# Optimization experiments

Measured on AMD Instinct MI355X. Metric: run time of the kernel, lower is better.

The kernel has to match this reference:

```python
import jax, jax.numpy as jnp
import numpy as np

N, E, F_IN, H, L = 50000, 800000, 128, 256, 3


def setup_inputs() -> dict:
    key = jax.random.key(0)
    ks = jax.random.split(key, 6)
    s = 0.05  # keep activations well-scaled through 3 residual layers
    return {
        "x": jax.random.normal(ks[0], (N, F_IN), jnp.float32),
        "edge_index": jax.random.randint(ks[1], (2, E), 0, N, dtype=jnp.int32),
        "Wp": jax.random.normal(ks[2], (H, F_IN), jnp.float32) * s,
        "bp": jnp.zeros((H,), jnp.float32),
        "Wl": jax.random.normal(ks[3], (L, H, H), jnp.float32) * s,
        "bl": jnp.zeros((L, H), jnp.float32),
        "Wr": jax.random.normal(ks[4], (L, H, H), jnp.float32) * s,
        "gamma": jnp.ones((L, H), jnp.float32),
        "beta": jnp.zeros((L, H), jnp.float32),
    }


def _layernorm(x, g, b, eps=1e-5):
    mu = jnp.mean(x, axis=-1, keepdims=True)
    var = jnp.var(x, axis=-1, keepdims=True)
    return (x - mu) * jax.lax.rsqrt(var + eps) * g + b


def reference(x, edge_index, Wp, bp, Wl, bl, Wr, gamma, beta):
    n = x.shape[0]
    src, dst = edge_index[0], edge_index[1]
    # input projection + ReLU
    h = jax.nn.relu(x @ Wp.T + bp)  # [N, H]
    # mean-aggregation normalizer (PyG SAGEConv 'mean'): zero-degree nodes -> 0
    deg = jax.ops.segment_sum(jnp.ones_like(dst, jnp.float32), dst, num_segments=n)
    inv_deg = (1.0 / jnp.maximum(deg, 1.0))[:, None]  # [N, 1]
    num_layers = Wl.shape[0]
    for i in range(num_layers):
        res = h
        # SAGEConv: lin_l(mean of source-neighbor messages) + lin_r(self)
        agg = jax.ops.segment_sum(h[src], dst, num_segments=n) * inv_deg  # [N, H]
        h = agg @ Wl[i].T + bl[i] + h @ Wr[i].T
        # LayerNorm -> ReLU -> (dropout: eval-mode identity) -> residual
        h = jax.nn.relu(_layernorm(h, gamma[i], beta[i])) + res
    return h
```

## Files before the change

### kernel.cpp

```cpp
#include <hip/hip_runtime.h>

#define NN 50000
#define EE 800000
#define FIN 128
#define HH 256
#define NL 3

#define BM 128
#define BK 32
#define TB (16384 + 8192)

typedef __bf16 bf16x8 __attribute__((ext_vector_type(8)));
typedef float  f32x4  __attribute__((ext_vector_type(4)));
typedef unsigned short u16x8 __attribute__((ext_vector_type(8)));

__device__ __forceinline__ float bf2f(unsigned short u){
    union { unsigned int i; float f; } v; v.i = ((unsigned int)u) << 16; return v.f;
}
__device__ __forceinline__ unsigned short f2bf(float f){
    union { float f; unsigned int i; } v; v.f = f;
    unsigned int r = v.i + 0x7FFF + ((v.i >> 16) & 1);
    return (unsigned short)(r >> 16);
}
__device__ __forceinline__ void gload16(const void* g, void* s){
    __builtin_amdgcn_global_load_lds(
        (const __attribute__((address_space(1))) void*)g,
        (__attribute__((address_space(3))) void*)s, 16, 0, 0);
}
__device__ __forceinline__ int permslot(int n){
    return (n & ~63) | ((n & 3) << 4) | ((n >> 2) & 15);
}

__global__ void k_zero_i32(int* __restrict__ p, int n){
    int i = blockIdx.x*256 + threadIdx.x;
    if (i < n) p[i] = 0;
}
__global__ void k_count_deg(const int* __restrict__ dst, int* __restrict__ deg){
    int i = blockIdx.x*256 + threadIdx.x;
    if (i < EE) atomicAdd(&deg[dst[i]], 1);
}
__global__ void k_block_sum(const int* __restrict__ deg, int* __restrict__ bsum){
    __shared__ int s[1024];
    int i = blockIdx.x*1024 + threadIdx.x;
    s[threadIdx.x] = (i < NN) ? deg[i] : 0;
    __syncthreads();
    for (int o = 512; o > 0; o >>= 1){
        if (threadIdx.x < o) s[threadIdx.x] += s[threadIdx.x + o];
        __syncthreads();
    }
    if (threadIdx.x == 0) bsum[blockIdx.x] = s[0];
}
__global__ void k_make_off(const int* __restrict__ deg, const int* __restrict__ bsum,
                           int nb, int* __restrict__ off, int* __restrict__ pos,
                           float* __restrict__ invd){
    __shared__ int s[1024];
    __shared__ int base;
    int t = threadIdx.x;
    if (t < 64){
        int v = (t < blockIdx.x && t < nb) ? bsum[t] : 0;
        #pragma unroll
        for (int m = 1; m <= 32; m <<= 1) v += __shfl_xor(v, m);
        if (t == 0) base = v;
    }
    int i = blockIdx.x*1024 + t;
    int v0 = (i < NN) ? deg[i] : 0;
    s[t] = v0; __syncthreads();
    for (int o = 1; o < 1024; o <<= 1){
        int add = (t >= o) ? s[t - o] : 0;
        __syncthreads();
        s[t] += add;
        __syncthreads();
    }
    if (i < NN){
        int excl = s[t] - v0 + base;
        off[i] = excl; pos[i] = excl;
        invd[i] = 1.0f / fmaxf((float)v0, 1.0f);
    }
}
__global__ __launch_bounds__(256) void k_build_csr(
    const int* __restrict__ src, const int* __restrict__ dst,
    int* __restrict__ pos, int* __restrict__ csr)
{
    const int grp = blockIdx.x & 7;
    const int bin = blockIdx.x >> 3;
    const int nbk = gridDim.x >> 3;
    const int lo  = grp * (NN/8);
    const int hi  = (grp == 7) ? NN : lo + (NN/8);
    for (int i = bin*256 + threadIdx.x; i < EE; i += nbk*256){
        int d = dst[i];
        if (d >= lo && d < hi){
            int p = atomicAdd(&pos[d], 1);
            csr[p] = src[i];
        }
    }
}

#define NX  (NN*FIN/4)
#define NWP (HH*FIN/4)
#define NWC (NL*HH*2*HH/4)
__global__ void k_prep(const float* __restrict__ x, const float* __restrict__ Wp,
                       const float* __restrict__ Wl, const float* __restrict__ Wr,
                       unsigned short* __restrict__ Xb, unsigned short* __restrict__ Wpb,
                       unsigned short* __restrict__ Wb){
    int i = blockIdx.x*256 + threadIdx.x;
    if (i < NX){
        float4 v = *(const float4*)&x[i*4];
        ushort4 o; o.x=f2bf(v.x); o.y=f2bf(v.y); o.z=f2bf(v.z); o.w=f2bf(v.w);
        *(ushort4*)&Xb[i*4] = o;
        return;
    }
    int j = i - NX;
    if (j < NWP){
        int base = j*4;
        int kk = base & (FIN-1);
        int n  = base >> 7;
        float4 v = *(const float4*)&Wp[base];
        ushort4 o; o.x=f2bf(v.x); o.y=f2bf(v.y); o.z=f2bf(v.z); o.w=f2bf(v.w);
        *(ushort4*)&Wpb[permslot(n)*FIN + kk] = o;
        return;
    }
    int k4 = j - NWP;
    if (k4 < NWC){
        int base = k4*4;
        int kk  = base & 511;
        int n   = (base >> 9) & (HH-1);
        int lyr = base >> 17;
        const float* srcp = (kk < HH) ? &Wl[((size_t)lyr*HH + n)*HH + kk]
                                      : &Wr[((size_t)lyr*HH + n)*HH + (kk - HH)];
        float4 v = *(const float4*)srcp;
        ushort4 o; o.x=f2bf(v.x); o.y=f2bf(v.y); o.z=f2bf(v.z); o.w=f2bf(v.w);
        *(ushort4*)&Wb[(size_t)lyr*HH*2*HH + permslot(n)*2*HH + kk] = o;
    }
}

__device__ __forceinline__ void accum16(float* a, uint4 v, float c){
    const unsigned int w0 = v.x, w1 = v.y, w2 = v.z, w3 = v.w;
    #pragma unroll
    for (int b = 0; b < 4; ++b){
        a[b]    += c * (float)((w0 >> (8*b)) & 0xFF);
        a[4+b]  += c * (float)((w1 >> (8*b)) & 0xFF);
        a[8+b]  += c * (float)((w2 >> (8*b)) & 0xFF);
        a[12+b] += c * (float)((w3 >> (8*b)) & 0xFF);
    }
}

__global__ __launch_bounds__(256) void k_aggregate_u8(
    const unsigned char* __restrict__ hu, const float* __restrict__ scl,
    const int* __restrict__ csr, const int* __restrict__ off,
    const int* __restrict__ deg, const float* __restrict__ invd,
    unsigned short* __restrict__ aggb)
{
    const int wave = threadIdx.x >> 6, lane = threadIdx.x & 63;
    const int node = blockIdx.x*4 + wave;
    if (node >= NN) return;
    const int o = off[node], d = deg[node];
    const int grp = lane >> 4;
    const int fl  = lane & 15;

    float acc[16] = {};
    int j = 0;
    for (; j + 16 <= d; j += 16){
        int s0 = csr[o + j      + grp];
        int s1 = csr[o + j + 4  + grp];
        int s2 = csr[o + j + 8  + grp];
        int s3 = csr[o + j + 12 + grp];
        float c0 = scl[s0], c1 = scl[s1], c2 = scl[s2], c3 = scl[s3];
        uint4 v0 = *(const uint4*)&hu[(size_t)s0*HH + fl*16];
        uint4 v1 = *(const uint4*)&hu[(size_t)s1*HH + fl*16];
        uint4 v2 = *(const uint4*)&hu[(size_t)s2*HH + fl*16];
        uint4 v3 = *(const uint4*)&hu[(size_t)s3*HH + fl*16];
        accum16(acc, v0, c0); accum16(acc, v1, c1);
        accum16(acc, v2, c2); accum16(acc, v3, c3);
    }
    for (; j + 8 <= d; j += 8){
        int s0 = csr[o + j     + grp];
        int s1 = csr[o + j + 4 + grp];
        float c0 = scl[s0], c1 = scl[s1];
        uint4 v0 = *(const uint4*)&hu[(size_t)s0*HH + fl*16];
        uint4 v1 = *(const uint4*)&hu[(size_t)s1*HH + fl*16];
        accum16(acc, v0, c0); accum16(acc, v1, c1);
    }
    for (; j < d; j += 4){
        int idx = j + grp;
        int s0 = 0; float c0 = 0.f;
        if (idx < d){ s0 = csr[o + idx]; c0 = scl[s0]; }
        uint4 v0 = *(const uint4*)&hu[(size_t)s0*HH + fl*16];
        accum16(acc, v0, c0);
    }
    #pragma unroll
    for (int k = 0; k < 16; ++k){
        acc[k] += __shfl_xor(acc[k], 16);
        acc[k] += __shfl_xor(acc[k], 32);
    }
    if (grp == 0){
        float id = invd[node];
        u16x8 r0, r1;
        #pragma unroll
        for (int k = 0; k < 8; ++k){
            r0[k] = f2bf(acc[k]*id);
            r1[k] = f2bf(acc[8+k]*id);
        }
        *(u16x8*)&aggb[(size_t)node*HH + fl*16]     = r0;
        *(u16x8*)&aggb[(size_t)node*HH + fl*16 + 8] = r1;
    }
}

template<int EPI>
__global__ __launch_bounds__(1024) void k_gemm_mfma(
    const unsigned short* __restrict__ A0, int lda0,
    const unsigned short* __restrict__ A1, int lda1,
    const unsigned short* __restrict__ Bt,
    const float* __restrict__ bias,
    const float* __restrict__ gamma, const float* __restrict__ beta,
    const unsigned short* __restrict__ resb,
    float* __restrict__ outf, unsigned short* __restrict__ outb,
    unsigned char* __restrict__ hu, float* __restrict__ scl,
    int K0, int KTOT)
{
    __shared__ char smem[3*TB];
    const int t    = threadIdx.x;
    const int w    = t >> 6, l = t & 63;
    const int lr   = l & 15, lg = l >> 4;
    const int half = w >> 3;
    const int wh   = w & 7;
    const int wm   = wh >> 2, wn = wh & 3;
    const int m0h  = blockIdx.x * BM + half*64;

    const int rowB = t >> 2;
    const int swzB = ((t & 3)*16) ^ ((rowB & 6) << 3);
    const char* bsrc = (const char*)(Bt + (size_t)rowB*KTOT) + swzB;
    const int bdstB = t*16;
    const int ua   = t & 255;
    const int rowA = ua >> 2;
    const int swzA = ((ua & 3)*16) ^ ((rowA & 6) << 3);
    int growA = m0h + rowA; if (growA > NN-1) growA = NN-1;
    const char* a0src = (const char*)(A0 + (size_t)growA*lda0) + swzA;
    const char* a1src = (const char*)(A1 + (size_t)growA*lda1) + swzA;
    const int adst = 16384 + half*4096 + ua*16;
    const bool hasA = (wh < 4);

    f32x4 acc[2][4] = {};

    auto stage = [&](int s, int buf){
        const int k0 = s * BK;
        char* base = smem + buf*TB;
        if (hasA){
            const char* g = (k0 < K0) ? (a0src + (size_t)k0*2)
                                      : (a1src + (size_t)(k0 - K0)*2);
            gload16(g, base + adst);
        }
        gload16(bsrc + (size_t)k0*2, base + bdstB);
    };

    const int nsteps = KTOT / BK;
    stage(0, 0);
    int buf = 0;
    for (int s = 0; s < nsteps; ++s){
        int nbuf = (buf == 2) ? 0 : buf + 1;
        if (s + 1 < nsteps){
            stage(s + 1, nbuf);
            if (hasA) { asm volatile("s_waitcnt vmcnt(2)" ::: "memory"); }
            else      { asm volatile("s_waitcnt vmcnt(1)" ::: "memory"); }
        } else {
            asm volatile("s_waitcnt vmcnt(0)" ::: "memory");
        }
        __builtin_amdgcn_s_barrier();
        __builtin_amdgcn_sched_barrier(0);

        const char* As = smem + buf*TB + 16384 + half*4096;
        const char* Bs = smem + buf*TB;
        const int kb = lg * 16;
        const int sw = (lr & 6) << 3;
        bf16x8 af[2], bfr[4];
        #pragma unroll
        for (int m = 0; m < 2; ++m){
            int r = wm*32 + m*16 + lr;
            af[m] = *(const bf16x8*)(As + r*64 + (kb ^ sw));
        }
        #pragma unroll
        for (int n = 0; n < 4; ++n){
            int r = wn*64 + n*16 + lr;
            bfr[n] = *(const bf16x8*)(Bs + r*64 + (kb ^ sw));
        }
        #pragma unroll
        for (int m = 0; m < 2; ++m)
            #pragma unroll
            for (int n = 0; n < 4; ++n)
                acc[m][n] = __builtin_amdgcn_mfma_f32_16x16x32_bf16(af[m], bfr[n], acc[m][n], 0, 0, 0);

        buf = nbuf;
    }
    __syncthreads();

    const int cb = wn*64 + lr*4;
    float4 bq = *(const float4*)&bias[cb];
    float bcol[4] = {bq.x, bq.y, bq.z, bq.w};
    float gcol[4], becol[4];
    if (EPI >= 1){
        float4 gq = *(const float4*)&gamma[cb];
        float4 eq = *(const float4*)&beta[cb];
        gcol[0]=gq.x; gcol[1]=gq.y; gcol[2]=gq.z; gcol[3]=gq.w;
        becol[0]=eq.x; becol[1]=eq.y; becol[2]=eq.z; becol[3]=eq.w;
    }

    float* red  = (float*)(smem + half*4096);
    float* red2 = red + 512;
    float pmx[2][4];

    if (EPI == 0){
        #pragma unroll
        for (int m = 0; m < 2; ++m)
        #pragma unroll
        for (int reg = 0; reg < 4; ++reg){
            int R = wm*32 + m*16 + lg*4 + reg;
            int grow = m0h + R;
            float mx = 0.f;
            ushort4 hb4;
            #pragma unroll
            for (int n = 0; n < 4; ++n){
                float v = fmaxf(acc[m][n][reg] + bcol[n], 0.f);
                acc[m][n][reg] = v;
                mx = fmaxf(mx, v);
                ((unsigned short*)&hb4)[n] = f2bf(v);
            }
            if (grow < NN) *(ushort4*)&outb[(size_t)grow*HH + cb] = hb4;
            pmx[m][reg] = mx;
        }
    } else {
        float sm[2][4], sq[2][4];
        #pragma unroll
        for (int m = 0; m < 2; ++m)
        #pragma unroll
        for (int reg = 0; reg < 4; ++reg){
            float s = 0.f, q = 0.f;
            #pragma unroll
            for (int n = 0; n < 4; ++n){
                float v = acc[m][n][reg] + bcol[n];
                acc[m][n][reg] = v;
                s += v; q += v*v;
            }
            sm[m][reg] = s; sq[m][reg] = q;
        }
        #pragma unroll
        for (int mask = 1; mask <= 8; mask <<= 1){
            #pragma unroll
            for (int m = 0; m < 2; ++m)
            #pragma unroll
            for (int reg = 0; reg < 4; ++reg){
                sm[m][reg] += __shfl_xor(sm[m][reg], mask);
                sq[m][reg] += __shfl_xor(sq[m][reg], mask);
            }
        }
        if (lr == 0){
            #pragma unroll
            for (int m = 0; m < 2; ++m)
            #pragma unroll
            for (int reg = 0; reg < 4; ++reg){
                int R = wm*32 + m*16 + lg*4 + reg;
                red[(wn*64 + R)*2 + 0] = sm[m][reg];
                red[(wn*64 + R)*2 + 1] = sq[m][reg];
            }
        }
        __syncthreads();
        #pragma unroll
        for (int m = 0; m < 2; ++m)
        #pragma unroll
        for (int reg = 0; reg < 4; ++reg){
            int R = wm*32 + m*16 + lg*4 + reg;
            float S = 0.f, Q = 0.f;
            #pragma unroll
            for (int ww = 0; ww < 4; ++ww){
                S += red[(ww*64 + R)*2 + 0];
                Q += red[(ww*64 + R)*2 + 1];
            }
            float mean = S * (1.0f/HH);
            float var  = Q * (1.0f/HH) - mean*mean;
            float inv  = rsqrtf(var + 1e-5f);
            int grow = m0h + R;
            int growc = (grow > NN-1) ? NN-1 : grow;
            ushort4 rv = *(const ushort4*)&resb[(size_t)growc*HH + cb];
            float mx = 0.f;
            ushort4 hb4;
            f32x4 fo;
            #pragma unroll
            for (int n = 0; n < 4; ++n){
                float o = fmaxf((acc[m][n][reg] - mean)*inv*gcol[n] + becol[n], 0.f)
                          + bf2f(((const unsigned short*)&rv)[n]);
                acc[m][n][reg] = o;
                mx = fmaxf(mx, o);
                if (EPI == 1) ((unsigned short*)&hb4)[n] = f2bf(o);
                else          fo[n] = o;
            }
            if (grow < NN){
                if (EPI == 1) *(ushort4*)&outb[(size_t)grow*HH + cb] = hb4;
                else          *(f32x4*)&outf[(size_t)grow*HH + cb] = fo;
            }
            pmx[m][reg] = mx;
        }
    }

    if (EPI <= 1){
        #pragma unroll
        for (int mask = 1; mask <= 8; mask <<= 1){
            #pragma unroll
            for (int m = 0; m < 2; ++m)
            #pragma unroll
            for (int reg = 0; reg < 4; ++reg)
                pmx[m][reg] = fmaxf(pmx[m][reg], __shfl_xor(pmx[m][reg], mask));
        }
        if (EPI == 0) __syncthreads();
        if (lr == 0){
            #pragma unroll
            for (int m = 0; m < 2; ++m)
            #pragma unroll
            for (int reg = 0; reg < 4; ++reg){
                int R = wm*32 + m*16 + lg*4 + reg;
                red2[wn*64 + R] = pmx[m][reg];
            }
        }
        __syncthreads();
        #pragma unroll
        for (int m = 0; m < 2; ++m)
        #pragma unroll
        for (int reg = 0; reg < 4; ++reg){
            int R = wm*32 + m*16 + lg*4 + reg;
            float rmax = fmaxf(fmaxf(red2[R], red2[64 + R]),
                               fmaxf(red2[128 + R], red2[192 + R]));
            float qinv = (rmax > 0.f) ? (255.0f / rmax) : 0.f;
            int grow = m0h + R;
            if (grow >= NN) continue;
            unsigned int q4 = 0;
            #pragma unroll
            for (int n = 0; n < 4; ++n){
                unsigned int qv = (unsigned int)(acc[m][n][reg]*qinv + 0.5f);
                q4 |= qv << (8*n);
            }
            *(unsigned int*)&hu[(size_t)grow*HH + cb] = q4;
            if (wn == 0 && lr == 0) scl[grow] = rmax * (1.0f/255.0f);
        }
    }
}

extern "C" void kernel_launch(void* const* d_in, const int* in_sizes, int n_in,
                              void* d_out, int out_size, void* d_ws, size_t ws_size,
                              hipStream_t stream) {
    const float* x     = (const float*)d_in[0];
    const int*   ei    = (const int*)d_in[1];
    const int*   srcI  = ei;
    const int*   dstI  = ei + EE;
    const float* Wp    = (const float*)d_in[2];
    const float* bp    = (const float*)d_in[3];
    const float* Wl    = (const float*)d_in[4];
    const float* bl    = (const float*)d_in[5];
    const float* Wr    = (const float*)d_in[6];
    const float* gamma = (const float*)d_in[7];
    const float* beta  = (const float*)d_in[8];
    float* out = (float*)d_out;

    char* ws = (char*)d_ws;
    size_t off_b = 0;
    auto alloc = [&](size_t bytes) -> char* {
        char* p = ws + off_b;
        off_b = (off_b + bytes + 255) & ~(size_t)255;
        return p;
    };
    unsigned short* Hb0  = (unsigned short*)alloc((size_t)NN*HH*2);
    unsigned short* Hb1  = (unsigned short*)alloc((size_t)NN*HH*2);
    unsigned short* AGGb = (unsigned short*)alloc((size_t)NN*HH*2);
    unsigned char*  Hu0  = (unsigned char*)alloc((size_t)NN*HH);
    unsigned char*  Hu1  = (unsigned char*)alloc((size_t)NN*HH);
    float* Scl0 = (float*)alloc((size_t)NN*4);
    float* Scl1 = (float*)alloc((size_t)NN*4);
    unsigned short* Xb = (unsigned short*)alloc((size_t)NN*FIN*2);
    int*   csr  = (int*)alloc((size_t)EE*4);
    int*   deg  = (int*)alloc((size_t)NN*4);
    int*   offs = (int*)alloc((size_t)NN*4);
    int*   pos  = (int*)alloc((size_t)NN*4);
    float* invd = (float*)alloc((size_t)NN*4);
    int*   bsum = (int*)alloc(64*4);
    unsigned short* Wpb = (unsigned short*)alloc((size_t)HH*FIN*2);
    unsigned short* Wb  = (unsigned short*)alloc((size_t)NL*HH*2*HH*2);
    (void)ws_size; (void)in_sizes; (void)n_in; (void)out_size;

    const int NB = (NN + 1023)/1024;

    k_zero_i32<<<(NN + 255)/256, 256, 0, stream>>>(deg, NN);
    k_count_deg<<<(EE + 255)/256, 256, 0, stream>>>(dstI, deg);
    k_block_sum<<<NB, 1024, 0, stream>>>(deg, bsum);
    k_make_off<<<NB, 1024, 0, stream>>>(deg, bsum, NB, offs, pos, invd);
    k_prep<<<(NX + NWP + NWC + 255)/256, 256, 0, stream>>>(x, Wp, Wl, Wr, Xb, Wpb, Wb);
    k_build_csr<<<1024, 256, 0, stream>>>(srcI, dstI, pos, csr);

    const int GB = (NN + BM - 1)/BM;

    k_gemm_mfma<0><<<GB, 1024, 0, stream>>>(Xb, FIN, Xb, FIN, Wpb, bp,
                                            nullptr, nullptr, nullptr,
                                            nullptr, Hb0, Hu0, Scl0,
                                            FIN, FIN);

    unsigned short* hin = Hb0;
    unsigned char*  huin = Hu0;
    float*          sclin = Scl0;
    for (int lyr = 0; lyr < NL; ++lyr){
        k_aggregate_u8<<<(NN + 3)/4, 256, 0, stream>>>(huin, sclin, csr, offs, deg,
                                                       invd, AGGb);
        unsigned short* hout  = (hin == Hb0) ? Hb1 : Hb0;
        unsigned char*  huout = (huin == Hu0) ? Hu1 : Hu0;
        float*          sclout= (sclin == Scl0) ? Scl1 : Scl0;
        const unsigned short* Wbt = Wb + (size_t)lyr*HH*2*HH;
        if (lyr < NL-1)
            k_gemm_mfma<1><<<GB, 1024, 0, stream>>>(AGGb, HH, hin, HH, Wbt, bl + lyr*HH,
                                                    gamma + lyr*HH, beta + lyr*HH, hin,
                                                    nullptr, hout, huout, sclout,
                                                    HH, 2*HH);
        else
            k_gemm_mfma<2><<<GB, 1024, 0, stream>>>(AGGb, HH, hin, HH, Wbt, bl + lyr*HH,
                                                    gamma + lyr*HH, beta + lyr*HH, hin,
                                                    out, nullptr, nullptr, nullptr,
                                                    HH, 2*HH);
        hin = hout; huin = huout; sclin = sclout;
    }
}
```

Measured before the change: 341.5 us.

## Enlarge GEMM tile to 256 rows with 8 waves per block computing 128x64 each

The fused GEMM+LayerNorm kernel moves from 1024-thread blocks that split two independent 64-row halves to 512-thread blocks that each own a full 256-row tile. Each wave now accumulates 8x4 MFMA tiles, so every loaded B fragment is reused across more rows and B tile traffic per output row drops. The epilogue reductions are restructured to match, and the launch bounds target two blocks per CU. The larger accumulator array (128 fp32 per lane) raises register pressure, and halving the block count may reduce load balance across CUs.

After: 354.0 us. 1.04x slower.

```diff
diff --git a/kernel.cpp b/kernel.cpp
--- a/kernel.cpp
+++ b/kernel.cpp
@@ -6,9 +6,9 @@
 #define HH 256
 #define NL 3
 
-#define BM 128
+#define BM 256
 #define BK 32
-#define TB (16384 + 8192)
+#define TB 32768
 
 typedef __bf16 bf16x8 __attribute__((ext_vector_type(8)));
 typedef float  f32x4  __attribute__((ext_vector_type(4)));
@@ -206,7 +206,7 @@
 }
 
 template<int EPI>
-__global__ __launch_bounds__(1024) void k_gemm_mfma(
+__global__ __launch_bounds__(512, 2) void k_gemm_mfma(
     const unsigned short* __restrict__ A0, int lda0,
     const unsigned short* __restrict__ A1, int lda1,
     const unsigned short* __restrict__ Bt,
@@ -218,38 +218,47 @@
     int K0, int KTOT)
 {
     __shared__ char smem[3*TB];
-    const int t    = threadIdx.x;
-    const int w    = t >> 6, l = t & 63;
-    const int lr   = l & 15, lg = l >> 4;
-    const int half = w >> 3;
-    const int wh   = w & 7;
-    const int wm   = wh >> 2, wn = wh & 3;
-    const int m0h  = blockIdx.x * BM + half*64;
-
-    const int rowB = t >> 2;
-    const int swzB = ((t & 3)*16) ^ ((rowB & 6) << 3);
-    const char* bsrc = (const char*)(Bt + (size_t)rowB*KTOT) + swzB;
-    const int bdstB = t*16;
-    const int ua   = t & 255;
-    const int rowA = ua >> 2;
-    const int swzA = ((ua & 3)*16) ^ ((rowA & 6) << 3);
-    int growA = m0h + rowA; if (growA > NN-1) growA = NN-1;
-    const char* a0src = (const char*)(A0 + (size_t)growA*lda0) + swzA;
-    const char* a1src = (const char*)(A1 + (size_t)growA*lda1) + swzA;
-    const int adst = 16384 + half*4096 + ua*16;
-    const bool hasA = (wh < 4);
-
-    f32x4 acc[2][4] = {};
+    const int t  = threadIdx.x;
+    const int w  = t >> 6, l = t & 63;
+    const int lr = l & 15, lg = l >> 4;
+    const int wm = w >> 2, wn = w & 3;
+    const int m0 = blockIdx.x * BM;
+
+    const char* bsrc[2]; int bdst[2];
+    #pragma unroll
+    for (int i = 0; i < 2; ++i){
+        int u   = t + i*512;
+        int row = u >> 2;
+        int swz = ((u & 3)*16) ^ ((row & 6) << 3);
+        bsrc[i] = (const char*)(Bt + (size_t)row*KTOT) + swz;
+        bdst[i] = u*16;
+    }
+    const char* asrc0[2]; const char* asrc1[2]; int adst[2];
+    #pragma unroll
+    for (int i = 0; i < 2; ++i){
+        int u   = t + i*512;
+        int row = u >> 2;
+        int swz = ((u & 3)*16) ^ ((row & 6) << 3);
+        int grow = m0 + row; if (grow > NN-1) grow = NN-1;
+        asrc0[i] = (const char*)(A0 + (size_t)grow*lda0) + swz;
+        asrc1[i] = (const char*)(A1 + (size_t)grow*lda1) + swz;
+        adst[i] = 16384 + u*16;
+    }
+
+    f32x4 acc[8][4] = {};
 
     auto stage = [&](int s, int buf){
         const int k0 = s * BK;
         char* base = smem + buf*TB;
-        if (hasA){
-            const char* g = (k0 < K0) ? (a0src + (size_t)k0*2)
-                                      : (a1src + (size_t)(k0 - K0)*2);
-            gload16(g, base + adst);
-        }
-        gload16(bsrc + (size_t)k0*2, base + bdstB);
+        gload16(bsrc[0] + (size_t)k0*2, base + bdst[0]);
+        gload16(bsrc[1] + (size_t)k0*2, base + bdst[1]);
+        if (k0 < K0){
+            gload16(asrc0[0] + (size_t)k0*2, base + adst[0]);
+            gload16(asrc0[1] + (size_t)k0*2, base + adst[1]);
+        } else {
+            gload16(asrc1[0] + (size_t)(k0 - K0)*2, base + adst[0]);
+            gload16(asrc1[1] + (size_t)(k0 - K0)*2, base + adst[1]);
+        }
     };
 
     const int nsteps = KTOT / BK;
@@ -259,22 +268,21 @@
         int nbuf = (buf == 2) ? 0 : buf + 1;
         if (s + 1 < nsteps){
             stage(s + 1, nbuf);
-            if (hasA) { asm volatile("s_waitcnt vmcnt(2)" ::: "memory"); }
-            else      { asm volatile("s_waitcnt vmcnt(1)" ::: "memory"); }
+            asm volatile("s_waitcnt vmcnt(4)" ::: "memory");
         } else {
             asm volatile("s_waitcnt vmcnt(0)" ::: "memory");
         }
         __builtin_amdgcn_s_barrier();
         __builtin_amdgcn_sched_barrier(0);
 
-        const char* As = smem + buf*TB + 16384 + half*4096;
         const char* Bs = smem + buf*TB;
+        const char* As = Bs + 16384;
         const int kb = lg * 16;
         const int sw = (lr & 6) << 3;
-        bf16x8 af[2], bfr[4];
-        #pragma unroll
-        for (int m = 0; m < 2; ++m){
-            int r = wm*32 + m*16 + lr;
+        bf16x8 af[8], bfr[4];
+        #pragma unroll
+        for (int m = 0; m < 8; ++m){
+            int r = wm*128 + m*16 + lr;
             af[m] = *(const bf16x8*)(As + r*64 + (kb ^ sw));
         }
         #pragma unroll
@@ -283,7 +291,7 @@
             bfr[n] = *(const bf16x8*)(Bs + r*64 + (kb ^ sw));
         }
         #pragma unroll
-        for (int m = 0; m < 2; ++m)
+        for (int m = 0; m < 8; ++m)
             #pragma unroll
             for (int n = 0; n < 4; ++n)
                 acc[m][n] = __builtin_amdgcn_mfma_f32_16x16x32_bf16(af[m], bfr[n], acc[m][n], 0, 0, 0);
@@ -303,17 +311,16 @@
         becol[0]=eq.x; becol[1]=eq.y; becol[2]=eq.z; becol[3]=eq.w;
     }
 
-    float* red  = (float*)(smem + half*4096);
-    float* red2 = red + 512;
-    float pmx[2][4];
+    float* red  = (float*)smem;
+    float* red2 = (float*)(smem + 8192);
 
     if (EPI == 0){
         #pragma unroll
-        for (int m = 0; m < 2; ++m)
+        for (int m = 0; m < 8; ++m)
         #pragma unroll
         for (int reg = 0; reg < 4; ++reg){
-            int R = wm*32 + m*16 + lg*4 + reg;
-            int grow = m0h + R;
+            int R = wm*128 + m*16 + lg*4 + reg;
+            int grow = m0 + R;
             float mx = 0.f;
             ushort4 hb4;
             #pragma unroll
@@ -324,14 +331,37 @@
                 ((unsigned short*)&hb4)[n] = f2bf(v);
             }
             if (grow < NN) *(ushort4*)&outb[(size_t)grow*HH + cb] = hb4;
-            pmx[m][reg] = mx;
+            #pragma unroll
+            for (int mask = 1; mask <= 8; mask <<= 1)
+                mx = fmaxf(mx, __shfl_xor(mx, mask));
+            if (lr == 0) red2[wn*256 + R] = mx;
+        }
+        __syncthreads();
+        #pragma unroll
+        for (int m = 0; m < 8; ++m)
+        #pragma unroll
+        for (int reg = 0; reg < 4; ++reg){
+            int R = wm*128 + m*16 + lg*4 + reg;
+            float rmax = fmaxf(fmaxf(red2[R], red2[256 + R]),
+                               fmaxf(red2[512 + R], red2[768 + R]));
+            float qinv = (rmax > 0.f) ? (255.0f / rmax) : 0.f;
+            int grow = m0 + R;
+            if (grow >= NN) continue;
+            unsigned int q4 = 0;
+            #pragma unroll
+            for (int n = 0; n < 4; ++n){
+                unsigned int qv = (unsigned int)(acc[m][n][reg]*qinv + 0.5f);
+                q4 |= qv << (8*n);
+            }
+            *(unsigned int*)&hu[(size_t)grow*HH + cb] = q4;
+            if (wn == 0 && lr == 0) scl[grow] = rmax * (1.0f/255.0f);
         }
     } else {
-        float sm[2][4], sq[2][4];
-        #pragma unroll
-        for (int m = 0; m < 2; ++m)
+        #pragma unroll
+        for (int m = 0; m < 8; ++m)
         #pragma unroll
         for (int reg = 0; reg < 4; ++reg){
+            int R = wm*128 + m*16 + lg*4 + reg;
             float s = 0.f, q = 0.f;
             #pragma unroll
             for (int n = 0; n < 4; ++n){
@@ -339,44 +369,32 @@
                 acc[m][n][reg] = v;
                 s += v; q += v*v;
             }
-            sm[m][reg] = s; sq[m][reg] = q;
-        }
-        #pragma unroll
-        for (int mask = 1; mask <= 8; mask <<= 1){
-            #pragma unroll
-            for (int m = 0; m < 2; ++m)
-            #pragma unroll
-            for (int reg = 0; reg < 4; ++reg){
-                sm[m][reg] += __shfl_xor(sm[m][reg], mask);
-                sq[m][reg] += __shfl_xor(sq[m][reg], mask);
-            }
-        }
-        if (lr == 0){
-            #pragma unroll
-            for (int m = 0; m < 2; ++m)
-            #pragma unroll
-            for (int reg = 0; reg < 4; ++reg){
-                int R = wm*32 + m*16 + lg*4 + reg;
-                red[(wn*64 + R)*2 + 0] = sm[m][reg];
-                red[(wn*64 + R)*2 + 1] = sq[m][reg];
+            #pragma unroll
+            for (int mask = 1; mask <= 8; mask <<= 1){
+                s += __shfl_xor(s, mask);
+                q += __shfl_xor(q, mask);
+            }
+            if (lr == 0){
+                red[(wn*256 + R)*2 + 0] = s;
+                red[(wn*256 + R)*2 + 1] = q;
             }
         }
         __syncthreads();
         #pragma unroll
-        for (int m = 0; m < 2; ++m)
+        for (int m = 0; m < 8; ++m)
         #pragma unroll
         for (int reg = 0; reg < 4; ++reg){
-            int R = wm*32 + m*16 + lg*4 + reg;
+            int R = wm*128 + m*16 + lg*4 + reg;
             float S = 0.f, Q = 0.f;
             #pragma unroll
             for (int ww = 0; ww < 4; ++ww){
-                S += red[(ww*64 + R)*2 + 0];
-                Q += red[(ww*64 + R)*2 + 1];
+                S += red[(ww*256 + R)*2 + 0];
+                Q += red[(ww*256 + R)*2 + 1];
             }
             float mean = S * (1.0f/HH);
             float var  = Q * (1.0f/HH) - mean*mean;
             float inv  = rsqrtf(var + 1e-5f);
-            int grow = m0h + R;
+            int grow = m0 + R;
             int growc = (grow > NN-1) ? NN-1 : grow;
             ushort4 rv = *(const ushort4*)&resb[(size_t)growc*HH + cb];
             float mx = 0.f;
@@ -395,48 +413,34 @@
                 if (EPI == 1) *(ushort4*)&outb[(size_t)grow*HH + cb] = hb4;
                 else          *(f32x4*)&outf[(size_t)grow*HH + cb] = fo;
             }
-            pmx[m][reg] = mx;
-        }
-    }
-
-    if (EPI <= 1){
-        #pragma unroll
-        for (int mask = 1; mask <= 8; mask <<= 1){
-            #pragma unroll
-            for (int m = 0; m < 2; ++m)
-            #pragma unroll
-            for (int reg = 0; reg < 4; ++reg)
-                pmx[m][reg] = fmaxf(pmx[m][reg], __shfl_xor(pmx[m][reg], mask));
-        }
-        if (EPI == 0) __syncthreads();
-        if (lr == 0){
-            #pragma unroll
-            for (int m = 0; m < 2; ++m)
+            if (EPI == 1){
+                #pragma unroll
+                for (int mask = 1; mask <= 8; mask <<= 1)
+                    mx = fmaxf(mx, __shfl_xor(mx, mask));
+                if (lr == 0) red2[wn*256 + R] = mx;
+            }
+        }
+        if (EPI == 1){
+            __syncthreads();
+            #pragma unroll
+            for (int m = 0; m < 8; ++m)
             #pragma unroll
             for (int reg = 0; reg < 4; ++reg){
-                int R = wm*32 + m*16 + lg*4 + reg;
-                red2[wn*64 + R] = pmx[m][reg];
-            }
-        }
-        __syncthreads();
-        #pragma unroll
-        for (int m = 0; m < 2; ++m)
-        #pragma unroll
-        for (int reg = 0; reg < 4; ++reg){
-            int R = wm*32 + m*16 + lg*4 + reg;
-            float rmax = fmaxf(fmaxf(red2[R], red2[64 + R]),
-                               fmaxf(red2[128 + R], red2[192 + R]));
-            float qinv = (rmax > 0.f) ? (255.0f / rmax) : 0.f;
-            int grow = m0h + R;
-            if (grow >= NN) continue;
-            unsigned int q4 = 0;
-            #pragma unroll
-            for (int n = 0; n < 4; ++n){
-                unsigned int qv = (unsigned int)(acc[m][n][reg]*qinv + 0.5f);
-                q4 |= qv << (8*n);
-            }
-            *(unsigned int*)&hu[(size_t)grow*HH + cb] = q4;
-            if (wn == 0 && lr == 0) scl[grow] = rmax * (1.0f/255.0f);
+                int R = wm*128 + m*16 + lg*4 + reg;
+                float rmax = fmaxf(fmaxf(red2[R], red2[256 + R]),
+                                   fmaxf(red2[512 + R], red2[768 + R]));
+                float qinv = (rmax > 0.f) ? (255.0f / rmax) : 0.f;
+                int grow = m0 + R;
+                if (grow >= NN) continue;
+                unsigned int q4 = 0;
+                #pragma unroll
+                for (int n = 0; n < 4; ++n){
+                    unsigned int qv = (unsigned int)(acc[m][n][reg]*qinv + 0.5f);
+                    q4 |= qv << (8*n);
+                }
+                *(unsigned int*)&hu[(size_t)grow*HH + cb] = q4;
+                if (wn == 0 && lr == 0) scl[grow] = rmax * (1.0f/255.0f);
+            }
         }
     }
 }
@@ -493,10 +497,10 @@
 
     const int GB = (NN + BM - 1)/BM;
 
-    k_gemm_mfma<0><<<GB, 1024, 0, stream>>>(Xb, FIN, Xb, FIN, Wpb, bp,
-                                            nullptr, nullptr, nullptr,
-                                            nullptr, Hb0, Hu0, Scl0,
-                                            FIN, FIN);
+    k_gemm_mfma<0><<<GB, 512, 0, stream>>>(Xb, FIN, Xb, FIN, Wpb, bp,
+                                           nullptr, nullptr, nullptr,
+                                           nullptr, Hb0, Hu0, Scl0,
+                                           FIN, FIN);
 
     unsigned short* hin = Hb0;
     unsigned char*  huin = Hu0;
@@ -509,15 +513,15 @@
         float*          sclout= (sclin == Scl0) ? Scl1 : Scl0;
         const unsigned short* Wbt = Wb + (size_t)lyr*HH*2*HH;
         if (lyr < NL-1)
-            k_gemm_mfma<1><<<GB, 1024, 0, stream>>>(AGGb, HH, hin, HH, Wbt, bl + lyr*HH,
-                                                    gamma + lyr*HH, beta + lyr*HH, hin,
-                                                    nullptr, hout, huout, sclout,
-                                                    HH, 2*HH);
+            k_gemm_mfma<1><<<GB, 512, 0, stream>>>(AGGb, HH, hin, HH, Wbt, bl + lyr*HH,
+                                                   gamma + lyr*HH, beta + lyr*HH, hin,
+                                                   nullptr, hout, huout, sclout,
+                                                   HH, 2*HH);
         else
-            k_gemm_mfma<2><<<GB, 1024, 0, stream>>>(AGGb, HH, hin, HH, Wbt, bl + lyr*HH,
-                                                    gamma + lyr*HH, beta + lyr*HH, hin,
-                                                    out, nullptr, nullptr, nullptr,
-                                                    HH, 2*HH);
+            k_gemm_mfma<2><<<GB, 512, 0, stream>>>(AGGb, HH, hin, HH, Wbt, bl + lyr*HH,
+                                                   gamma + lyr*HH, beta + lyr*HH, hin,
+                                                   out, nullptr, nullptr, nullptr,
+                                                   HH, 2*HH);
         hin = hout; huin = huout; sclin = sclout;
     }
 }
```
